# Kernel tuning notes

Hardware: AMD Instinct MI355X
Metric: run time of the kernel (lower is better)

Reference implementation:

```python
import jax, jax.numpy as jnp
import numpy as np

VOCAB = 32000
WDIM = 768      # bert-base hidden size, per self.w_dim
H = 512         # lstm_hidden
NUM_CAT = 5
START = 3       # l2ind['SOS']
END = 4         # l2ind['EOS']
T = 2048
NEG = -10000.0


def _lstm_dir(x, Wih, Whh, bih, bhh, reverse):
    # x: [T, WDIM]; torch LSTM gate order: i, f, g, o
    z_in = x @ Wih.T + bih + bhh  # [T, 4H] precompute input projection
    def step(carry, zt):
        h, c = carry
        z = zt + h @ Whh.T
        i, f, g, o = jnp.split(z, 4)
        c = jax.nn.sigmoid(f) * c + jax.nn.sigmoid(i) * jnp.tanh(g)
        h = jax.nn.sigmoid(o) * jnp.tanh(c)
        return (h, c), h
    init = (jnp.zeros((H,), x.dtype), jnp.zeros((H,), x.dtype))
    _, hs = jax.lax.scan(step, init, z_in, reverse=reverse)
    return hs  # [T, H], aligned with input order


def setup_inputs():
    key = jax.random.key(0)
    ks = jax.random.split(key, 13)
    s = 0.05
    sent = jax.random.randint(ks[0], (T,), 0, VOCAB)
    emb = jax.random.normal(ks[1], (VOCAB, WDIM), jnp.float32) * 0.02
    Wih_f = jax.random.normal(ks[2], (4 * H, WDIM), jnp.float32) * s
    Whh_f = jax.random.normal(ks[3], (4 * H, H), jnp.float32) * s
    bih_f = jax.random.normal(ks[4], (4 * H,), jnp.float32) * s
    bhh_f = jax.random.normal(ks[5], (4 * H,), jnp.float32) * s
    Wih_b = jax.random.normal(ks[6], (4 * H, WDIM), jnp.float32) * s
    Whh_b = jax.random.normal(ks[7], (4 * H, H), jnp.float32) * s
    bih_b = jax.random.normal(ks[8], (4 * H,), jnp.float32) * s
    bhh_b = jax.random.normal(ks[9], (4 * H,), jnp.float32) * s
    fc_w = jax.random.normal(ks[10], (NUM_CAT, 2 * H), jnp.float32) * s
    fc_b = jax.random.normal(ks[11], (NUM_CAT,), jnp.float32) * s
    transitions = jax.random.normal(ks[12], (NUM_CAT, NUM_CAT), jnp.float32)
    transitions = transitions.at[START, :].set(NEG).at[:, END].set(NEG)
    return {"sent": sent, "emb": emb,
            "Wih_f": Wih_f, "Whh_f": Whh_f, "bih_f": bih_f, "bhh_f": bhh_f,
            "Wih_b": Wih_b, "Whh_b": Whh_b, "bih_b": bih_b, "bhh_b": bhh_b,
            "fc_w": fc_w, "fc_b": fc_b, "transitions": transitions}


def reference(sent, emb, Wih_f, Whh_f, bih_f, bhh_f, Wih_b, Whh_b, bih_b, bhh_b, fc_w, fc_b, transitions):
    # _get_scores: embedding -> BiLSTM -> fc
    x = emb[sent]                                   # [T, WDIM]
    h_f = _lstm_dir(x, Wih_f, Whh_f, bih_f, bhh_f, reverse=False)
    h_b = _lstm_dir(x, Wih_b, Whh_b, bih_b, bhh_b, reverse=True)
    out = jnp.concatenate([h_f, h_b], axis=-1)      # [T, 2H]
    feats = out @ fc_w.T + fc_b                     # [T, NUM_CAT]

    # _viterbi_decode: transitions[i, j] = score of moving from tag j to tag i
    init = feats[0] + transitions[:, START]         # [NUM_CAT]
    def vstep(layer, feat_t):
        # scores[i, j] = feat_t[i] + transitions[i, j] + layer[j]
        scores = feat_t[:, None] + transitions + layer[None, :]
        return jnp.max(scores, axis=1), jnp.argmax(scores, axis=1)
    layer, parents = jax.lax.scan(vstep, init, feats[1:])  # parents: [T-1, NUM_CAT]

    final = layer + transitions[END]
    idx0 = jnp.argmax(final)
    path_score = jnp.max(final)

    # backtrack (parents[0] of the original loop is all-START and gets popped)
    def btrack(idx, p):
        nxt = p[idx]
        return nxt, nxt
    _, idxs = jax.lax.scan(btrack, idx0, parents, reverse=True)  # [T-1]
    path = jnp.concatenate([idxs, idx0[None]])      # [T]
    return path, path_score
```

## Files before the change

kernel.cpp:

```cpp
#include <hip/hip_runtime.h>

#define TT 2048
#define WD 768
#define HH 512
#define G4 2048
#define NC 5
#define SENT 0xFFFFFFFFu

typedef float f4 __attribute__((ext_vector_type(4)));

__global__ __launch_bounds__(256) void zin_gemm(
    const int* __restrict__ sent, const float* __restrict__ emb,
    const float* __restrict__ Wih_f, const float* __restrict__ bih_f, const float* __restrict__ bhh_f,
    const float* __restrict__ Wih_b, const float* __restrict__ bih_b, const float* __restrict__ bhh_b,
    float* __restrict__ zin_f, float* __restrict__ zin_b)
{
    const int dirn = blockIdx.z;
    const float* Wih = dirn ? Wih_b : Wih_f;
    const float* bih = dirn ? bih_b : bih_f;
    const float* bhh = dirn ? bhh_b : bhh_f;
    float* zin = dirn ? zin_b : zin_f;

    __shared__ float As[16][128];
    __shared__ float Bs[16][128];

    const int tid = threadIdx.x;
    const int t0 = blockIdx.y * 128;
    const int g0 = blockIdx.x * 128;
    const int tm = tid >> 4, tn = tid & 15;

    float acc[8][8];
#pragma unroll
    for (int a = 0; a < 8; a++)
#pragma unroll
        for (int b = 0; b < 8; b++) acc[a][b] = 0.f;

    for (int kt = 0; kt < 48; ++kt) {
        const int k0 = kt * 16;
#pragma unroll
        for (int u = 0; u < 2; ++u) {
            const int s = tid * 2 + u;
            const int m = s >> 2, kq = s & 3;
            const int rowA = sent[t0 + m];
            float4 av = *(const float4*)(emb + (size_t)rowA * WD + k0 + kq * 4);
            As[kq * 4 + 0][m] = av.x; As[kq * 4 + 1][m] = av.y;
            As[kq * 4 + 2][m] = av.z; As[kq * 4 + 3][m] = av.w;
            float4 bv = *(const float4*)(Wih + (size_t)(g0 + m) * WD + k0 + kq * 4);
            Bs[kq * 4 + 0][m] = bv.x; Bs[kq * 4 + 1][m] = bv.y;
            Bs[kq * 4 + 2][m] = bv.z; Bs[kq * 4 + 3][m] = bv.w;
        }
        __syncthreads();
#pragma unroll
        for (int kk = 0; kk < 16; ++kk) {
            float4 a0 = *(const float4*)&As[kk][tm * 8];
            float4 a1 = *(const float4*)&As[kk][tm * 8 + 4];
            float4 b0 = *(const float4*)&Bs[kk][tn * 8];
            float4 b1 = *(const float4*)&Bs[kk][tn * 8 + 4];
            float av8[8] = {a0.x, a0.y, a0.z, a0.w, a1.x, a1.y, a1.z, a1.w};
            float bv8[8] = {b0.x, b0.y, b0.z, b0.w, b1.x, b1.y, b1.z, b1.w};
#pragma unroll
            for (int a = 0; a < 8; a++)
#pragma unroll
                for (int b = 0; b < 8; b++) acc[a][b] += av8[a] * bv8[b];
        }
        __syncthreads();
    }
    float bias[8];
#pragma unroll
    for (int b = 0; b < 8; b++) { int g = g0 + tn * 8 + b; bias[b] = bih[g] + bhh[g]; }
#pragma unroll
    for (int a = 0; a < 8; a++) {
        const int t = t0 + tm * 8 + a;
        float* op = zin + (size_t)t * G4 + g0 + tn * 8;
        float4 o0 = {acc[a][0] + bias[0], acc[a][1] + bias[1], acc[a][2] + bias[2], acc[a][3] + bias[3]};
        float4 o1 = {acc[a][4] + bias[4], acc[a][5] + bias[5], acc[a][6] + bias[6], acc[a][7] + bias[7]};
        *(float4*)op = o0; *(float4*)(op + 4) = o1;
    }
}

__global__ __launch_bounds__(256, 1) void lstm_rec(
    const float* __restrict__ zin_f, const float* __restrict__ zin_b,
    const float* __restrict__ Whh_f, const float* __restrict__ Whh_b,
    unsigned int* __restrict__ hw_f, unsigned int* __restrict__ hw_b)
{
    const int bid = blockIdx.x;
    const int d = bid >> 5;
    const int k = bid & 31;
    const float* zin = d ? zin_b : zin_f;
    const float* Whh = d ? Whh_b : Whh_f;
    unsigned int* hw = d ? hw_b : hw_f;

    const int tid = threadIdx.x;
    const int q = tid >> 6;
    const int r = tid & 63;
    const int gate = r >> 4, jj = r & 15;
    const int grow = gate * HH + k * 16 + jj;

    const f4* wp = (const f4*)(Whh + (size_t)grow * HH + q * 128);
    f4 w[32];
#pragma unroll
    for (int i = 0; i < 32; ++i) w[i] = wp[i];
#pragma unroll
    for (int i = 0; i < 32; ++i)
        asm volatile("" : "+v"(w[i]));

    __shared__ float hs[HH];
    __shared__ float zb[256];

    float c = 0.f;
    const int n = k * 16 + tid;
    const int s2 = tid * 2;

    for (int it = 0; it < TT; ++it) {
        const int t = d ? (TT - 1 - it) : it;

        float z0 = 0, z1 = 0, z2 = 0, z3 = 0;
        if (tid < 16) {
            const float* zt = zin + (size_t)t * G4 + n;
            z0 = zt[0]; z1 = zt[512]; z2 = zt[1024]; z3 = zt[1536];
        }

        if (it > 0) {
            const int tp = d ? (t + 1) : (t - 1);
            const unsigned long long* hq =
                (const unsigned long long*)(hw + (size_t)tp * HH + s2);
            unsigned long long v;
            do {
                v = __hip_atomic_load(hq, __ATOMIC_RELAXED, __HIP_MEMORY_SCOPE_AGENT);
            } while ((unsigned int)v == SENT || (unsigned int)(v >> 32) == SENT);
            hs[s2]     = __uint_as_float((unsigned int)v);
            hs[s2 + 1] = __uint_as_float((unsigned int)(v >> 32));
        }
        __syncthreads();

        float part = 0.f;
        if (it > 0) {
            const f4* hv = ((const f4*)hs) + (q << 5);
#pragma unroll
            for (int i = 0; i < 32; ++i) {
                f4 h4 = hv[i];
                part += w[i].x * h4.x + w[i].y * h4.y + w[i].z * h4.z + w[i].w * h4.w;
            }
        }
        zb[tid] = part;
        __syncthreads();

        if (tid < 16) {
            float s0 = 0, s1 = 0, sg = 0, s3 = 0;
#pragma unroll
            for (int qq = 0; qq < 4; ++qq) {
                const int b = qq * 64 + tid;
                s0 += zb[b]; s1 += zb[b + 16]; sg += zb[b + 32]; s3 += zb[b + 48];
            }
            const float gi = 1.f / (1.f + expf(-(z0 + s0)));
            const float gf = 1.f / (1.f + expf(-(z1 + s1)));
            const float gg = tanhf(z2 + sg);
            const float go = 1.f / (1.f + expf(-(z3 + s3)));
            c = gf * c + gi * gg;
            const float hval = go * tanhf(c);
            __hip_atomic_store(&hw[(size_t)t * HH + n], __float_as_uint(hval),
                               __ATOMIC_RELAXED, __HIP_MEMORY_SCOPE_AGENT);
        }
    }
}

__global__ void feats_kernel(const float* __restrict__ h_f, const float* __restrict__ h_b,
                             const float* __restrict__ fc_w, const float* __restrict__ fc_b,
                             float* __restrict__ feats)
{
    const int t = blockIdx.x;
    const int l = threadIdx.x;
    float acc[NC] = {0.f, 0.f, 0.f, 0.f, 0.f};
    for (int m = 0; m < 16; ++m) {
        const int cg = l + m * 64;
        const float hv = (cg < HH) ? h_f[(size_t)t * HH + cg]
                                   : h_b[(size_t)t * HH + cg - HH];
#pragma unroll
        for (int i = 0; i < NC; i++) acc[i] += hv * fc_w[i * (2 * HH) + cg];
    }
#pragma unroll
    for (int i = 0; i < NC; i++) {
#pragma unroll
        for (int off = 32; off; off >>= 1) acc[i] += __shfl_xor(acc[i], off);
    }
    if (l == 0) {
#pragma unroll
        for (int i = 0; i < NC; i++) feats[(size_t)t * NC + i] = acc[i] + fc_b[i];
    }
}

__global__ void viterbi_kernel(const float* __restrict__ feats,
                               const float* __restrict__ trans,
                               float* __restrict__ out)
{
    __shared__ float fs[TT * NC];
    __shared__ int par[TT];
    __shared__ float pathv[TT];
    const int tid = threadIdx.x;
    for (int i = tid; i < TT * NC; i += 64) fs[i] = feats[i];
    float tr[25];
#pragma unroll
    for (int i = 0; i < 25; i++) tr[i] = trans[i];
    __syncthreads();

    float layer[NC];
#pragma unroll
    for (int i = 0; i < NC; i++) layer[i] = fs[i] + tr[i * 5 + 3];

    for (int s = 0; s < TT - 1; ++s) {
        const float* ft = &fs[(s + 1) * NC];
        float nl[NC]; int pk = 0;
#pragma unroll
        for (int i = 0; i < NC; i++) {
            float best = tr[i * 5 + 0] + layer[0]; int bj = 0;
#pragma unroll
            for (int jj = 1; jj < NC; jj++) {
                const float v = tr[i * 5 + jj] + layer[jj];
                if (v > best) { best = v; bj = jj; }
            }
            nl[i] = ft[i] + best;
            pk |= bj << (3 * i);
        }
#pragma unroll
        for (int i = 0; i < NC; i++) layer[i] = nl[i];
        if (tid == 0) par[s] = pk;
    }
    float best = layer[0] + tr[20]; int idx0 = 0;
#pragma unroll
    for (int jj = 1; jj < NC; jj++) {
        const float v = layer[jj] + tr[20 + jj];
        if (v > best) { best = v; idx0 = jj; }
    }
    __syncthreads();
    if (tid == 0) {
        pathv[TT - 1] = (float)idx0;
        int idx = idx0;
        for (int s = TT - 2; s >= 0; --s) {
            idx = (par[s] >> (3 * idx)) & 7;
            pathv[s] = (float)idx;
        }
        out[TT] = best;
    }
    __syncthreads();
    for (int i = tid; i < TT; i += 64) out[i] = pathv[i];
}

extern "C" void kernel_launch(void* const* d_in, const int* in_sizes, int n_in,
                              void* d_out, int out_size, void* d_ws, size_t ws_size,
                              hipStream_t stream) {
    const int*   sent   = (const int*)d_in[0];
    const float* emb    = (const float*)d_in[1];
    const float* Wih_f  = (const float*)d_in[2];
    const float* Whh_f  = (const float*)d_in[3];
    const float* bih_f  = (const float*)d_in[4];
    const float* bhh_f  = (const float*)d_in[5];
    const float* Wih_b  = (const float*)d_in[6];
    const float* Whh_b  = (const float*)d_in[7];
    const float* bih_b  = (const float*)d_in[8];
    const float* bhh_b  = (const float*)d_in[9];
    const float* fc_w   = (const float*)d_in[10];
    const float* fc_b   = (const float*)d_in[11];
    const float* trans  = (const float*)d_in[12];
    float* out = (float*)d_out;

    char* ws = (char*)d_ws;
    float* zin_f = (float*)ws;
    float* zin_b = (float*)(ws + (size_t)16777216);
    unsigned int* hw_f = (unsigned int*)(ws + (size_t)33554432);
    unsigned int* hw_b = (unsigned int*)(ws + (size_t)37748736);
    float* feats = (float*)(ws + (size_t)41943040);

    hipMemsetAsync(hw_f, 0xFF, (size_t)8388608, stream);

    dim3 gg(G4 / 128, TT / 128, 2);
    zin_gemm<<<gg, 256, 0, stream>>>(sent, emb, Wih_f, bih_f, bhh_f,
                                     Wih_b, bih_b, bhh_b, zin_f, zin_b);

    lstm_rec<<<64, 256, 0, stream>>>(zin_f, zin_b, Whh_f, Whh_b, hw_f, hw_b);

    feats_kernel<<<TT, 64, 0, stream>>>((const float*)hw_f, (const float*)hw_b,
                                        fc_w, fc_b, feats);

    viterbi_kernel<<<1, 64, 0, stream>>>(feats, trans, out);
}
```

Baseline: 5.649 ms.

## Poll recurrent h with wide cache-bypassing loads and parallelize gate activations

The recurrent LSTM kernel now has a single wavefront poll for the previous hidden state. Each lane spins on two dwordx4 loads issued with sc0 sc1 cache-bypass bits, replacing per-thread 64-bit atomic loads spread across all 256 threads. Gate activations are computed by 64 lanes in parallel (one gate element each) and gathered with shuffles, instead of 16 lanes each doing four transcendentals. Recurrent weights are pinned in AGPRs to free VGPRs, at the cost of extra accumulator-to-vector moves each step.

```diff
diff --git a/kernel.cpp b/kernel.cpp
--- a/kernel.cpp
+++ b/kernel.cpp
@@ -8,6 +8,7 @@
 #define SENT 0xFFFFFFFFu
 
 typedef float f4 __attribute__((ext_vector_type(4)));
+typedef unsigned int u4 __attribute__((ext_vector_type(4)));
 
 __global__ __launch_bounds__(256) void zin_gemm(
     const int* __restrict__ sent, const float* __restrict__ emb,
@@ -102,36 +103,42 @@
     for (int i = 0; i < 32; ++i) w[i] = wp[i];
 #pragma unroll
     for (int i = 0; i < 32; ++i)
-        asm volatile("" : "+v"(w[i]));
+        asm volatile("" : "+a"(w[i]));
 
     __shared__ float hs[HH];
     __shared__ float zb[256];
 
     float c = 0.f;
-    const int n = k * 16 + tid;
-    const int s2 = tid * 2;
+    const int l = tid;
+    const int g = l >> 4, j = l & 15;
+    const int n16 = k * 16 + j;
 
     for (int it = 0; it < TT; ++it) {
         const int t = d ? (TT - 1 - it) : it;
 
-        float z0 = 0, z1 = 0, z2 = 0, z3 = 0;
-        if (tid < 16) {
-            const float* zt = zin + (size_t)t * G4 + n;
-            z0 = zt[0]; z1 = zt[512]; z2 = zt[1024]; z3 = zt[1536];
-        }
-
-        if (it > 0) {
+        float z = 0.f;
+        if (tid < 64) z = zin[(size_t)t * G4 + g * HH + n16];
+
+        if (it > 0 && tid < 64) {
             const int tp = d ? (t + 1) : (t - 1);
-            const unsigned long long* hq =
-                (const unsigned long long*)(hw + (size_t)tp * HH + s2);
-            unsigned long long v;
-            do {
-                v = __hip_atomic_load(hq, __ATOMIC_RELAXED, __HIP_MEMORY_SCOPE_AGENT);
-            } while ((unsigned int)v == SENT || (unsigned int)(v >> 32) == SENT);
-            hs[s2]     = __uint_as_float((unsigned int)v);
-            hs[s2 + 1] = __uint_as_float((unsigned int)(v >> 32));
-        }
-        __syncthreads();
+            const unsigned int* pa = hw + (size_t)tp * HH + l * 8;
+            u4 a0, a1;
+            for (;;) {
+                asm volatile(
+                    "global_load_dwordx4 %0, %2, off sc0 sc1\n\t"
+                    "global_load_dwordx4 %1, %2, off offset:16 sc0 sc1\n\t"
+                    "s_waitcnt vmcnt(0)"
+                    : "=v"(a0), "=v"(a1) : "v"(pa) : "memory");
+                if (a0.x != SENT && a0.y != SENT && a0.z != SENT && a0.w != SENT &&
+                    a1.x != SENT && a1.y != SENT && a1.z != SENT && a1.w != SENT) break;
+            }
+            u4* hd = (u4*)(hs + l * 8);
+            hd[0] = a0; hd[1] = a1;
+        }
+        __syncthreads();
+
+#pragma unroll
+        for (int i = 0; i < 32; ++i) asm volatile("" : "+a"(w[i]));
 
         float part = 0.f;
         if (it > 0) {
@@ -145,21 +152,23 @@
         zb[tid] = part;
         __syncthreads();
 
-        if (tid < 16) {
-            float s0 = 0, s1 = 0, sg = 0, s3 = 0;
-#pragma unroll
-            for (int qq = 0; qq < 4; ++qq) {
-                const int b = qq * 64 + tid;
-                s0 += zb[b]; s1 += zb[b + 16]; sg += zb[b + 32]; s3 += zb[b + 48];
-            }
-            const float gi = 1.f / (1.f + expf(-(z0 + s0)));
-            const float gf = 1.f / (1.f + expf(-(z1 + s1)));
-            const float gg = tanhf(z2 + sg);
-            const float go = 1.f / (1.f + expf(-(z3 + s3)));
-            c = gf * c + gi * gg;
-            const float hval = go * tanhf(c);
-            __hip_atomic_store(&hw[(size_t)t * HH + n], __float_as_uint(hval),
-                               __ATOMIC_RELAXED, __HIP_MEMORY_SCOPE_AGENT);
+        if (tid < 64) {
+            float s = zb[l] + zb[64 + l] + zb[128 + l] + zb[192 + l];
+            const float pre = z + s;
+            float act;
+            if (g == 2) act = tanhf(pre);
+            else        act = 1.f / (1.f + expf(-pre));
+            const float gi = __shfl(act, j);
+            const float gf = __shfl(act, j + 16);
+            const float gg = __shfl(act, j + 32);
+            const float go = __shfl(act, j + 48);
+            if (l < 16) {
+                c = gf * c + gi * gg;
+                const float hval = go * tanhf(c);
+                __hip_atomic_store(&hw[(size_t)t * HH + k * 16 + l],
+                                   __float_as_uint(hval),
+                                   __ATOMIC_RELAXED, __HIP_MEMORY_SCOPE_AGENT);
+            }
         }
     }
 }
```

Result: faster. 4.769 ms (-15.6%).
